# Kernel tuning notes

Hardware: AMD Instinct MI355X
Metric: run time of the kernel (lower is better)

Reference implementation:

```python
import jax, jax.numpy as jnp
import numpy as np
import math

B, S, D, H = 4, 2048, 1024, 16
HD = D // H
MASKED_BIAS = -10000.0

def setup_inputs() -> dict:
    key = jax.random.key(0)
    k1, k2, k3, k4, k5 = jax.random.split(key, 5)
    scale = 0.02
    return {
        "hidden_states": jax.random.normal(k1, (B, S, D), dtype=jnp.float32),
        "w_attn": jax.random.normal(k2, (D, 3 * D), dtype=jnp.float32) * scale,
        "b_attn": jnp.zeros((3 * D,), dtype=jnp.float32),
        "w_proj": jax.random.normal(k3, (D, D), dtype=jnp.float32) * scale,
        "b_proj": jnp.zeros((D,), dtype=jnp.float32),
    }

def reference(hidden_states, w_attn, b_attn, w_proj, b_proj):
    b, s, d = hidden_states.shape
    qkv = hidden_states @ w_attn + b_attn                      # [B,S,3D]
    q, k, v = jnp.split(qkv, 3, axis=-1)
    # split heads -> [B,H,S,HD]
    def split_heads(x):
        return x.reshape(b, s, H, HD).transpose(0, 2, 1, 3)
    q, k, v = split_heads(q), split_heads(k), split_heads(v)
    scores = jnp.einsum("bhqd,bhkd->bhqk", q, k) / math.sqrt(HD)
    causal = jnp.tril(jnp.ones((s, s), dtype=bool))
    scores = jnp.where(causal[None, None], scores, jnp.float32(MASKED_BIAS))
    probs = jax.nn.softmax(scores, axis=-1)
    ctx = jnp.einsum("bhqk,bhkd->bhqd", probs, v)
    ctx = ctx.transpose(0, 2, 1, 3).reshape(b, s, d)           # merge heads
    return ctx @ w_proj + b_proj
```

## Files before the change

### kernel.cpp

```cpp
#include <hip/hip_runtime.h>

typedef unsigned short u16;
typedef __attribute__((ext_vector_type(8))) short short8;
typedef __attribute__((ext_vector_type(4))) float f32x4;
typedef __attribute__((ext_vector_type(4))) unsigned u32x4;

#define Bq 4
#define Sq 2048
#define Dq 1024
#define Hq 16
#define HDq 64
#define BSq 8192

#define QSCALE 0.18033688011112042f

__device__ __forceinline__ u16 f2bf(float f) {
  unsigned u = __builtin_bit_cast(unsigned, f);
  unsigned r = u + 0x7fffu + ((u >> 16) & 1u);
  return (u16)(r >> 16);
}

__device__ __forceinline__ unsigned pk2(float a, float b) {
  unsigned ua = __builtin_bit_cast(unsigned, a) + 0x8000u;
  unsigned ub = __builtin_bit_cast(unsigned, b) + 0x8000u;
  return __builtin_amdgcn_perm(ub, ua, 0x07060302u);
}

__device__ __forceinline__ unsigned cvtpk(float a, float b) {
  unsigned r;
  asm("v_cvt_pk_bf16_f32 %0, %1, %2" : "=v"(r) : "v"(a), "v"(b));
  return r;
}

__device__ __forceinline__ void gl_lds16(const u16* g, u16* l) {
  __builtin_amdgcn_global_load_lds((const __attribute__((address_space(1))) unsigned int*)g,
                                   (__attribute__((address_space(3))) unsigned int*)l, 16, 0, 0);
}

__device__ __forceinline__ int kperm(int kk) {
  return ((kk & 0x10) << 1) | ((kk & 0x0C) << 1) | ((kk & 0x20) >> 3) | (kk & 3);
}

__global__ void cvt_kernel(const float* __restrict__ in, u16* __restrict__ out, int n8) {
  int i = blockIdx.x * blockDim.x + threadIdx.x;
  if (i >= n8) return;
  float4 v0 = reinterpret_cast<const float4*>(in)[2 * i];
  float4 v1 = reinterpret_cast<const float4*>(in)[2 * i + 1];
  u32x4 o;
  o[0] = pk2(v0.x, v0.y); o[1] = pk2(v0.z, v0.w);
  o[2] = pk2(v1.x, v1.y); o[3] = pk2(v1.z, v1.w);
  reinterpret_cast<u32x4*>(out)[i] = o;
}

__global__ void transpose_cvt(const float* __restrict__ in, u16* __restrict__ out, int R, int C) {
  __shared__ float tile[32][33];
  int c0 = blockIdx.x * 32, r0 = blockIdx.y * 32;
  for (int i = threadIdx.y; i < 32; i += 8)
    tile[i][threadIdx.x] = in[(size_t)(r0 + i) * C + c0 + threadIdx.x];
  __syncthreads();
  for (int i = threadIdx.y; i < 32; i += 8)
    out[(size_t)(c0 + i) * R + r0 + threadIdx.x] = f2bf(tile[threadIdx.x][i]);
}

template<int EPI>
__global__ __launch_bounds__(256)
void gemm_bt(const u16* __restrict__ A, const u16* __restrict__ Bt,
             const float* __restrict__ bias,
             u16* __restrict__ Qb, u16* __restrict__ Kb, u16* __restrict__ Vt,
             float* __restrict__ Out, int Kdim) {
  __shared__ __align__(16) u16 As[128 * 64];
  __shared__ __align__(16) u16 Bs[128 * 64];
  int tid = threadIdx.x;
  int lane = tid & 63;
  int wid = tid >> 6;
  int wr = wid >> 1, wc = wid & 1;
  constexpr int NX = (EPI == 0) ? 24 : 8;
  constexpr int NWG = NX * 64;
  int orig = (int)blockIdx.x + NX * (int)blockIdx.y;
  int swz = (orig & 7) * (NWG >> 3) + (orig >> 3);
  int m0 = (swz / NX) * 128, n0 = (swz % NX) * 128;
  int l15 = lane & 15, g = lane >> 4;
  f32x4 acc[4][4] = {};

  const u16* aP[4];
  const u16* bP[4];
#pragma unroll
  for (int i = 0; i < 4; ++i) {
    int f = i * 256 + tid;
    int row = f >> 3, slot = f & 7;
    int src = ((slot ^ (row & 7)) << 3);
    aP[i] = &A[(size_t)(m0 + row) * Kdim + src];
    bP[i] = &Bt[(size_t)(n0 + row) * Kdim + src];
  }

  int nk = Kdim >> 6;
  for (int t = 0; t < nk; ++t) {
    __syncthreads();
    int ko = t << 6;
#pragma unroll
    for (int i = 0; i < 4; ++i) {
      int f = i * 256 + tid;
      gl_lds16(aP[i] + ko, &As[f << 3]);
      gl_lds16(bP[i] + ko, &Bs[f << 3]);
    }
    __syncthreads();
#pragma unroll
    for (int ksub = 0; ksub < 2; ++ksub) {
      int sl = (((ksub << 2) | g) ^ (l15 & 7)) << 3;
      short8 af[4], bfr[4];
#pragma unroll
      for (int m = 0; m < 4; ++m)
        af[m] = *reinterpret_cast<const short8*>(&As[(wr * 64 + m * 16 + l15) * 64 + sl]);
#pragma unroll
      for (int n = 0; n < 4; ++n)
        bfr[n] = *reinterpret_cast<const short8*>(&Bs[(wc * 64 + n * 16 + l15) * 64 + sl]);
      __builtin_amdgcn_s_setprio(1);
#pragma unroll
      for (int m = 0; m < 4; ++m)
#pragma unroll
        for (int n = 0; n < 4; ++n)
          acc[m][n] = __builtin_amdgcn_mfma_f32_16x16x32_bf16(af[m], bfr[n], acc[m][n], 0, 0, 0);
      __builtin_amdgcn_s_setprio(0);
    }
  }

  int bb = (m0 + wr * 64) >> 11;
  int sb = (m0 + wr * 64) & 2047;

  if (EPI == 1) {
#pragma unroll
    for (int m = 0; m < 4; ++m)
#pragma unroll
      for (int n = 0; n < 4; ++n) {
        int gcol = n0 + wc * 64 + n * 16 + l15;
        float bv = bias[gcol];
#pragma unroll
        for (int r = 0; r < 4; ++r) {
          int grow = m0 + wr * 64 + m * 16 + g * 4 + r;
          Out[(size_t)grow * 1024 + gcol] = acc[m][n][r] + bv;
        }
      }
  } else if (n0 < 1024) {
#pragma unroll
    for (int n = 0; n < 4; ++n) {
      int col = n0 + wc * 64 + n * 16 + l15;
      int hh = col >> 6, d = col & 63;
      float bv = bias[col];
      u16* qb = &Qb[(((size_t)(bb * 16 + hh) * 2048 + sb) << 6) + d];
#pragma unroll
      for (int m = 0; m < 4; ++m)
#pragma unroll
        for (int r = 0; r < 4; ++r)
          qb[(size_t)(m * 16 + g * 4 + r) << 6] = f2bf((acc[m][n][r] + bv) * QSCALE);
    }
  } else if (n0 < 2048) {
#pragma unroll
    for (int n = 0; n < 4; ++n) {
      int col = n0 - 1024 + wc * 64 + n * 16 + l15;
      int hh = col >> 6, d = col & 63;
      float bv = bias[1024 + col];
      u16* kb = &Kb[(((size_t)(bb * 16 + hh) * 2048 + sb) << 6) + d];
#pragma unroll
      for (int m = 0; m < 4; ++m)
#pragma unroll
        for (int r = 0; r < 4; ++r)
          kb[(size_t)(m * 16 + g * 4 + r) << 6] = f2bf(acc[m][n][r] + bv);
    }
  } else {
#pragma unroll
    for (int n = 0; n < 4; ++n) {
      int cc = n0 - 2048 + wc * 64 + n * 16 + l15;
      int hh = cc >> 6, d = cc & 63;
      float bv = bias[2048 + cc];
      u16* dst = &Vt[((size_t)(bb * 16 + hh) * 64 + d) * 2048 + sb];
      u32x4 lo, hi;
      lo[0] = pk2(acc[0][n][0] + bv, acc[0][n][1] + bv);
      lo[1] = pk2(acc[0][n][2] + bv, acc[0][n][3] + bv);
      lo[2] = pk2(acc[2][n][0] + bv, acc[2][n][1] + bv);
      lo[3] = pk2(acc[2][n][2] + bv, acc[2][n][3] + bv);
      hi[0] = pk2(acc[1][n][0] + bv, acc[1][n][1] + bv);
      hi[1] = pk2(acc[1][n][2] + bv, acc[1][n][3] + bv);
      hi[2] = pk2(acc[3][n][0] + bv, acc[3][n][1] + bv);
      hi[3] = pk2(acc[3][n][2] + bv, acc[3][n][3] + bv);
      *reinterpret_cast<u32x4*>(dst + g * 8) = lo;
      *reinterpret_cast<u32x4*>(dst + 32 + g * 8) = hi;
    }
  }
}

__global__ __launch_bounds__(256, 2)
void attn_kernel(const u16* __restrict__ Qb, const u16* __restrict__ Kb,
                 const u16* __restrict__ Vt, u16* __restrict__ Ctx) {
  __shared__ __align__(16) u16 lds[2][2][8][512];
  int tid = threadIdx.x, lane = tid & 63, w = tid >> 6;
  int l15 = lane & 15, g = lane >> 4;
  int bh = blockIdx.y;
  const u16* Qh = Qb + (size_t)bh * Sq * HDq;
  const u16* Kh = Kb + (size_t)bh * Sq * HDq;
  const u16* Vh = Vt + (size_t)bh * HDq * Sq;
  int b = bh >> 4, h = bh & 15;

  int qb = 15 - (int)blockIdx.x;
  int nk = 2 * qb + 2;
  int qbase = qb * 128 + w * 32;

  const u16* ksrc = Kh + (size_t)(16 * w + l15) * 64 + 8 * g;
  const u16* vsrc = Vh + (size_t)(16 * w + l15) * Sq + 8 * g;
  const u16* kpre = ksrc + 4096;
  const u16* vpre = vsrc + 64;

  short8 qf[2][2];
#pragma unroll
  for (int s = 0; s < 2; ++s)
#pragma unroll
    for (int hh = 0; hh < 2; ++hh)
      qf[s][hh] = *reinterpret_cast<const short8*>(&Qh[(size_t)(qbase + 16 * s + l15) * 64 + 32 * hh + 8 * g]);

  u16 onebits = (l15 == 0) ? (u16)0x3F80 : (u16)0;
  short8 vones;
#pragma unroll
  for (int i = 0; i < 8; ++i) vones[i] = (short)onebits;

  f32x4 acc[2][4] = {};
  f32x4 acc_l[2] = {};

  gl_lds16(ksrc,      &lds[0][0][2 * w][0]);
  gl_lds16(ksrc + 32, &lds[0][0][2 * w + 1][0]);
  gl_lds16(vsrc,      &lds[0][1][2 * w][0]);
  gl_lds16(vsrc + 32, &lds[0][1][2 * w + 1][0]);
  __syncthreads();
  int cur = 0;

#pragma unroll 1
  for (int kb = 0; kb < nk; ++kb) {
    int k0 = kb << 6;

    if (kb + 1 < nk) {
      gl_lds16(kpre,      &lds[cur ^ 1][0][2 * w][0]);
      gl_lds16(kpre + 32, &lds[cur ^ 1][0][2 * w + 1][0]);
      gl_lds16(vpre,      &lds[cur ^ 1][1][2 * w][0]);
      gl_lds16(vpre + 32, &lds[cur ^ 1][1][2 * w + 1][0]);
      kpre += 4096; vpre += 64;
    }

    short8 kf[4][2], vbf[4][2];
#pragma unroll
    for (int j = 0; j < 4; ++j) {
      kf[j][0] = *reinterpret_cast<const short8*>(&lds[cur][0][2 * j][lane * 8]);
      kf[j][1] = *reinterpret_cast<const short8*>(&lds[cur][0][2 * j + 1][lane * 8]);
    }
#pragma unroll
    for (int n = 0; n < 4; ++n) {
      vbf[n][0] = *reinterpret_cast<const short8*>(&lds[cur][1][2 * n][lane * 8]);
      vbf[n][1] = *reinterpret_cast<const short8*>(&lds[cur][1][2 * n + 1][lane * 8]);
    }

#pragma unroll
    for (int s = 0; s < 2; ++s) {
      int q0s = qbase + 16 * s;

      f32x4 sj[4];
      __builtin_amdgcn_s_setprio(1);
#pragma unroll
      for (int j = 0; j < 4; ++j) {
        f32x4 z = {};
        z = __builtin_amdgcn_mfma_f32_16x16x32_bf16(kf[j][0], qf[s][0], z, 0, 0, 0);
        z = __builtin_amdgcn_mfma_f32_16x16x32_bf16(kf[j][1], qf[s][1], z, 0, 0, 0);
        sj[j] = z;
      }
      __builtin_amdgcn_s_setprio(0);

      if (k0 + 63 > q0s) {
        int q = q0s + l15;
#pragma unroll
        for (int j = 0; j < 4; ++j)
#pragma unroll
          for (int r = 0; r < 4; ++r)
            if (k0 + 16 * j + 4 * g + r > q) sj[j][r] = -1e30f;
      }

      float p[4][4];
#pragma unroll
      for (int j = 0; j < 4; ++j)
#pragma unroll
        for (int r = 0; r < 4; ++r)
          p[j][r] = exp2f(sj[j][r]);

      u32x4 w0, w1;
      w0[0] = cvtpk(p[0][0], p[0][1]); w0[1] = cvtpk(p[0][2], p[0][3]);
      w0[2] = cvtpk(p[2][0], p[2][1]); w0[3] = cvtpk(p[2][2], p[2][3]);
      w1[0] = cvtpk(p[1][0], p[1][1]); w1[1] = cvtpk(p[1][2], p[1][3]);
      w1[2] = cvtpk(p[3][0], p[3][1]); w1[3] = cvtpk(p[3][2], p[3][3]);
      short8 pa0 = __builtin_bit_cast(short8, w0);
      short8 pa1 = __builtin_bit_cast(short8, w1);
      __builtin_amdgcn_s_setprio(1);
#pragma unroll
      for (int n = 0; n < 4; ++n) {
        acc[s][n] = __builtin_amdgcn_mfma_f32_16x16x32_bf16(pa0, vbf[n][0], acc[s][n], 0, 0, 0);
        acc[s][n] = __builtin_amdgcn_mfma_f32_16x16x32_bf16(pa1, vbf[n][1], acc[s][n], 0, 0, 0);
      }
      acc_l[s] = __builtin_amdgcn_mfma_f32_16x16x32_bf16(pa0, vones, acc_l[s], 0, 0, 0);
      acc_l[s] = __builtin_amdgcn_mfma_f32_16x16x32_bf16(pa1, vones, acc_l[s], 0, 0, 0);
      __builtin_amdgcn_s_setprio(0);
    }

    __syncthreads();
    cur ^= 1;
  }

#pragma unroll
  for (int s = 0; s < 2; ++s) {
    float lf[4];
#pragma unroll
    for (int r = 0; r < 4; ++r) lf[r] = __shfl(acc_l[s][r], 16 * g);
#pragma unroll
    for (int r = 0; r < 4; ++r) {
      float inv = 1.0f / lf[r];
      int row = qbase + 16 * s + 4 * g + r;
      size_t obase = ((size_t)(b * Sq + row)) * Dq + h * 64;
#pragma unroll
      for (int n = 0; n < 4; ++n)
        Ctx[obase + 16 * n + l15] = f2bf(acc[s][n][r] * inv);
    }
  }
}

extern "C" void kernel_launch(void* const* d_in, const int* in_sizes, int n_in,
                              void* d_out, int out_size, void* d_ws, size_t ws_size,
                              hipStream_t stream) {
  const float* X  = (const float*)d_in[0];
  const float* Wa = (const float*)d_in[1];
  const float* Ba = (const float*)d_in[2];
  const float* Wp = (const float*)d_in[3];
  const float* Bp = (const float*)d_in[4];
  float* Out = (float*)d_out;

  u16* ws  = (u16*)d_ws;
  u16* Xb  = ws;
  u16* WaT = Xb  + (size_t)BSq * Dq;
  u16* WpT = WaT + (size_t)3 * Dq * Dq;
  u16* Qb  = WpT + (size_t)Dq * Dq;
  u16* Kb  = Qb  + (size_t)Bq * Hq * Sq * HDq;
  u16* Vt  = Kb  + (size_t)Bq * Hq * Sq * HDq;
  u16* Ctx = Vt  + (size_t)Bq * Hq * Sq * HDq;

  cvt_kernel<<<(BSq * Dq / 8 + 255) / 256, 256, 0, stream>>>(X, Xb, BSq * Dq / 8);
  transpose_cvt<<<dim3(3 * Dq / 32, Dq / 32), dim3(32, 8), 0, stream>>>(Wa, WaT, Dq, 3 * Dq);
  transpose_cvt<<<dim3(Dq / 32, Dq / 32), dim3(32, 8), 0, stream>>>(Wp, WpT, Dq, Dq);
  gemm_bt<0><<<dim3(3 * Dq / 128, BSq / 128), 256, 0, stream>>>(Xb, WaT, Ba, Qb, Kb, Vt, nullptr, Dq);
  attn_kernel<<<dim3(16, Bq * Hq), 256, 0, stream>>>(Qb, Kb, Vt, Ctx);
  gemm_bt<1><<<dim3(Dq / 128, BSq / 128), 256, 0, stream>>>(Ctx, WpT, Bp, nullptr, nullptr, nullptr, Out, Dq);
}
```

Before: 206.3 us.

## Pair complementary causal query tiles per attention block for load balance

Each attention block now handles two 64-row query tiles, tile 31-x and tile x, with 128 threads instead of one 128-row tile with 256 threads. Every block therefore does the same total number of key-block iterations, which evens out the causal workload across blocks. The K/V prefetch pointer is reset when the first tile finishes, and the first tile's output is written out mid-loop. The cost is fewer waves per block and more global-to-LDS loads per wave, which may reduce latency hiding.

```diff
diff --git a/kernel.cpp b/kernel.cpp
--- a/kernel.cpp
+++ b/kernel.cpp
@@ -188,7 +188,7 @@
   }
 }
 
-__global__ __launch_bounds__(256, 2)
+__global__ __launch_bounds__(128, 2)
 void attn_kernel(const u16* __restrict__ Qb, const u16* __restrict__ Kb,
                  const u16* __restrict__ Vt, u16* __restrict__ Ctx) {
   __shared__ __align__(16) u16 lds[2][2][8][512];
@@ -200,21 +200,24 @@
   const u16* Vh = Vt + (size_t)bh * HDq * Sq;
   int b = bh >> 4, h = bh & 15;
 
-  int qb = 15 - (int)blockIdx.x;
-  int nk = 2 * qb + 2;
-  int qbase = qb * 128 + w * 32;
-
-  const u16* ksrc = Kh + (size_t)(16 * w + l15) * 64 + 8 * g;
-  const u16* vsrc = Vh + (size_t)(16 * w + l15) * Sq + 8 * g;
+  int tileA = 31 - (int)blockIdx.x, tileB = (int)blockIdx.x;
+  int nkA = tileA + 1;
+  int ntot = nkA + tileB + 1;
+
+  const u16* ksrc = Kh + (size_t)(32 * w + l15) * 64 + 8 * g;
+  const u16* vsrc = Vh + (size_t)(32 * w + l15) * Sq + 8 * g;
   const u16* kpre = ksrc + 4096;
   const u16* vpre = vsrc + 64;
 
+  int tile = tileA;
+  int qrow = tileA * 64 + 32 * w;
+
   short8 qf[2][2];
 #pragma unroll
   for (int s = 0; s < 2; ++s)
 #pragma unroll
     for (int hh = 0; hh < 2; ++hh)
-      qf[s][hh] = *reinterpret_cast<const short8*>(&Qh[(size_t)(qbase + 16 * s + l15) * 64 + 32 * hh + 8 * g]);
+      qf[s][hh] = *reinterpret_cast<const short8*>(&Qh[(size_t)(qrow + 16 * s + l15) * 64 + 32 * hh + 8 * g]);
 
   u16 onebits = (l15 == 0) ? (u16)0x3F80 : (u16)0;
   short8 vones;
@@ -224,23 +227,34 @@
   f32x4 acc[2][4] = {};
   f32x4 acc_l[2] = {};
 
-  gl_lds16(ksrc,      &lds[0][0][2 * w][0]);
-  gl_lds16(ksrc + 32, &lds[0][0][2 * w + 1][0]);
-  gl_lds16(vsrc,      &lds[0][1][2 * w][0]);
-  gl_lds16(vsrc + 32, &lds[0][1][2 * w + 1][0]);
+  gl_lds16(ksrc,         &lds[0][0][4 * w][0]);
+  gl_lds16(ksrc + 32,    &lds[0][0][4 * w + 1][0]);
+  gl_lds16(ksrc + 1024,  &lds[0][0][4 * w + 2][0]);
+  gl_lds16(ksrc + 1056,  &lds[0][0][4 * w + 3][0]);
+  gl_lds16(vsrc,         &lds[0][1][4 * w][0]);
+  gl_lds16(vsrc + 32,    &lds[0][1][4 * w + 1][0]);
+  gl_lds16(vsrc + 32768, &lds[0][1][4 * w + 2][0]);
+  gl_lds16(vsrc + 32800, &lds[0][1][4 * w + 3][0]);
   __syncthreads();
   int cur = 0;
+  int kb = 0;
 
 #pragma unroll 1
-  for (int kb = 0; kb < nk; ++kb) {
+  for (int it = 0; it < ntot; ++it) {
+    bool lastA = (it == nkA - 1);
     int k0 = kb << 6;
 
-    if (kb + 1 < nk) {
-      gl_lds16(kpre,      &lds[cur ^ 1][0][2 * w][0]);
-      gl_lds16(kpre + 32, &lds[cur ^ 1][0][2 * w + 1][0]);
-      gl_lds16(vpre,      &lds[cur ^ 1][1][2 * w][0]);
-      gl_lds16(vpre + 32, &lds[cur ^ 1][1][2 * w + 1][0]);
-      kpre += 4096; vpre += 64;
+    if (it + 1 < ntot) {
+      gl_lds16(kpre,         &lds[cur ^ 1][0][4 * w][0]);
+      gl_lds16(kpre + 32,    &lds[cur ^ 1][0][4 * w + 1][0]);
+      gl_lds16(kpre + 1024,  &lds[cur ^ 1][0][4 * w + 2][0]);
+      gl_lds16(kpre + 1056,  &lds[cur ^ 1][0][4 * w + 3][0]);
+      gl_lds16(vpre,         &lds[cur ^ 1][1][4 * w][0]);
+      gl_lds16(vpre + 32,    &lds[cur ^ 1][1][4 * w + 1][0]);
+      gl_lds16(vpre + 32768, &lds[cur ^ 1][1][4 * w + 2][0]);
+      gl_lds16(vpre + 32800, &lds[cur ^ 1][1][4 * w + 3][0]);
+      if (it == nkA - 2) { kpre = ksrc; vpre = vsrc; }
+      else               { kpre += 4096; vpre += 64; }
     }
 
     short8 kf[4][2], vbf[4][2];
@@ -257,7 +271,7 @@
 
 #pragma unroll
     for (int s = 0; s < 2; ++s) {
-      int q0s = qbase + 16 * s;
+      int q0s = qrow + 16 * s;
 
       f32x4 sj[4];
       __builtin_amdgcn_s_setprio(1);
@@ -270,7 +284,7 @@
       }
       __builtin_amdgcn_s_setprio(0);
 
-      if (k0 + 63 > q0s) {
+      if (kb == tile) {
         int q = q0s + l15;
 #pragma unroll
         for (int j = 0; j < 4; ++j)
@@ -304,23 +318,56 @@
       __builtin_amdgcn_s_setprio(0);
     }
 
+    kb++;
+    if (lastA) {
+#pragma unroll
+      for (int s = 0; s < 2; ++s) {
+        float lf[4];
+#pragma unroll
+        for (int r = 0; r < 4; ++r) lf[r] = __shfl(acc_l[s][r], 16 * g);
+#pragma unroll
+        for (int r = 0; r < 4; ++r) {
+          float inv = 1.0f / lf[r];
+          int row = qrow + 16 * s + 4 * g + r;
+          size_t obase = ((size_t)(b * Sq + row)) * Dq + h * 64;
+#pragma unroll
+          for (int n = 0; n < 4; ++n)
+            Ctx[obase + 16 * n + l15] = f2bf(acc[s][n][r] * inv);
+        }
+      }
+      qrow = tileB * 64 + 32 * w;
+      tile = tileB;
+      kb = 0;
+#pragma unroll
+      for (int s = 0; s < 2; ++s) {
+#pragma unroll
+        for (int hh = 0; hh < 2; ++hh)
+          qf[s][hh] = *reinterpret_cast<const short8*>(&Qh[(size_t)(qrow + 16 * s + l15) * 64 + 32 * hh + 8 * g]);
+#pragma unroll
+        for (int n = 0; n < 4; ++n) acc[s][n] = f32x4{};
+        acc_l[s] = f32x4{};
+      }
+    }
+
     __syncthreads();
     cur ^= 1;
   }
 
-#pragma unroll
-  for (int s = 0; s < 2; ++s) {
-    float lf[4];
-#pragma unroll
-    for (int r = 0; r < 4; ++r) lf[r] = __shfl(acc_l[s][r], 16 * g);
-#pragma unroll
-    for (int r = 0; r < 4; ++r) {
-      float inv = 1.0f / lf[r];
-      int row = qbase + 16 * s + 4 * g + r;
-      size_t obase = ((size_t)(b * Sq + row)) * Dq + h * 64;
-#pragma unroll
-      for (int n = 0; n < 4; ++n)
-        Ctx[obase + 16 * n + l15] = f2bf(acc[s][n][r] * inv);
+  {
+#pragma unroll
+    for (int s = 0; s < 2; ++s) {
+      float lf[4];
+#pragma unroll
+      for (int r = 0; r < 4; ++r) lf[r] = __shfl(acc_l[s][r], 16 * g);
+#pragma unroll
+      for (int r = 0; r < 4; ++r) {
+        float inv = 1.0f / lf[r];
+        int row = qrow + 16 * s + 4 * g + r;
+        size_t obase = ((size_t)(b * Sq + row)) * Dq + h * 64;
+#pragma unroll
+        for (int n = 0; n < 4; ++n)
+          Ctx[obase + 16 * n + l15] = f2bf(acc[s][n][r] * inv);
+      }
     }
   }
 }
@@ -348,6 +395,6 @@
   transpose_cvt<<<dim3(3 * Dq / 32, Dq / 32), dim3(32, 8), 0, stream>>>(Wa, WaT, Dq, 3 * Dq);
   transpose_cvt<<<dim3(Dq / 32, Dq / 32), dim3(32, 8), 0, stream>>>(Wp, WpT, Dq, Dq);
   gemm_bt<0><<<dim3(3 * Dq / 128, BSq / 128), 256, 0, stream>>>(Xb, WaT, Ba, Qb, Kb, Vt, nullptr, Dq);
-  attn_kernel<<<dim3(16, Bq * Hq), 256, 0, stream>>>(Qb, Kb, Vt, Ctx);
+  attn_kernel<<<dim3(16, Bq * Hq), 128, 0, stream>>>(Qb, Kb, Vt, Ctx);
   gemm_bt<1><<<dim3(Dq / 128, BSq / 128), 256, 0, stream>>>(Ctx, WpT, Bp, nullptr, nullptr, nullptr, Out, Dq);
 }
```

Result: faster. 184.1 us (-10.7%).
